# Optimization experiments

Measured on AMD Instinct MI355X. Metric: run time of the kernel, lower is better.

The kernel has to match this reference:

```python
import jax, jax.numpy as jnp
import numpy as np

N_G, E_G, E_H, E_I = 100000, 1000000, 1500000, 2000000
IN_FEATS = 64


def setup_inputs() -> dict:
    key = jax.random.key(0)
    ks = jax.random.split(key, 13)
    inp = {
        'z': jax.random.randint(ks[0], (N_G,), 0, 8),
        'src_g': jax.random.randint(ks[1], (E_G,), 0, N_G),
        'dst_g': jax.random.randint(ks[2], (E_G,), 0, N_G),
        'src_h': jax.random.randint(ks[3], (E_H,), 0, E_G),
        'dst_h': jax.random.randint(ks[4], (E_H,), 0, E_G),
        'src_i': jax.random.randint(ks[5], (E_I,), 0, E_H),
        'dst_i': jax.random.randint(ks[6], (E_I,), 0, E_H),
    }
    for n, k in zip(['e1', 'e2', 'e3', 'e4', 'e5', 'e6'], ks[7:13]):
        inp[n] = jax.random.normal(k, (2, IN_FEATS), dtype=jnp.float32)
    return inp


def reference(z, src_g, dst_g, src_h, dst_h, src_i, dst_i, e1, e2, e3, e4, e5, e6):
    # hop 1: g.apply_edges(send_z) -> per-edge endpoint labels, become h node data
    z_src = z[src_g]            # [E_G]
    z_dst = z[dst_g]            # [E_G]
    # hop 2: h.apply_edges(send_z2) -> become i node data
    z_src_src = z_src[src_h]    # [E_H]
    z_dst_dst = z_dst[dst_h]    # [E_H]
    # hop 3: i.apply_edges(comparison4) on edge endpoints of i
    za = z_src_src[src_i]       # [E_I]
    zb = z_src_src[dst_i]
    zc = z_dst_dst[src_i]
    zd = z_dst_dst[dst_i]
    zac = (za == zc).astype(jnp.int32)
    zab = (za == zb).astype(jnp.int32)
    zbc = (zc == zb).astype(jnp.int32)
    zad = (za == zd).astype(jnp.int32)
    zcd = (zc == zd).astype(jnp.int32)
    zbd = (zb == zd).astype(jnp.int32)
    # six 2-row embedding lookups summed -> [E_I, IN_FEATS]
    h = e1[zac] + e2[zab] + e3[zbc] + e4[zad] + e5[zcd] + e6[zbd]
    return h
```

## Files before the change

kernel.cpp:

```cpp
#include <hip/hip_runtime.h>


#define N_FEAT 64
#define WEPB   4096

typedef float f4 __attribute__((ext_vector_type(4)));

__global__ void hop1_table_kernel(const int* __restrict__ z,
                                  const int* __restrict__ src_g,
                                  const int* __restrict__ dst_g,
                                  unsigned short* __restrict__ zg,
                                  const float* __restrict__ e1,
                                  const float* __restrict__ e2,
                                  const float* __restrict__ e3,
                                  const float* __restrict__ e4,
                                  const float* __restrict__ e5,
                                  const float* __restrict__ e6,
                                  float* __restrict__ table,
                                  int n) {
    int i  = blockIdx.x * blockDim.x + threadIdx.x;
    int n4 = n >> 2;
    if (i < n4) {
        int4 s = ((const int4*)src_g)[i];
        int4 d = ((const int4*)dst_g)[i];
        unsigned zs0 = (unsigned)z[s.x], zd0 = (unsigned)z[d.x];
        unsigned zs1 = (unsigned)z[s.y], zd1 = (unsigned)z[d.y];
        unsigned zs2 = (unsigned)z[s.z], zd2 = (unsigned)z[d.z];
        unsigned zs3 = (unsigned)z[s.w], zd3 = (unsigned)z[d.w];
        unsigned r0 = (zs0 & 0xffu) | ((zd0 & 0xffu) << 8)
                    | ((zs1 & 0xffu) << 16) | ((zd1 & 0xffu) << 24);
        unsigned r1 = (zs2 & 0xffu) | ((zd2 & 0xffu) << 8)
                    | ((zs3 & 0xffu) << 16) | ((zd3 & 0xffu) << 24);
        ((uint2*)zg)[i] = make_uint2(r0, r1);
    } else {
        int e = (n4 << 2) + (i - n4);
        if (e < n) {
            zg[e] = (unsigned short)(((unsigned)z[src_g[e]] & 0xffu)
                                   | (((unsigned)z[dst_g[e]] & 0xffu) << 8));
        }
    }
    if (blockIdx.x < 16) {
        int idx = blockIdx.x * 256 + threadIdx.x;
        int cmb = idx >> 6;
        int f   = idx & (N_FEAT - 1);
        float v = e1[((cmb >> 0) & 1) * N_FEAT + f];
        v      += e2[((cmb >> 1) & 1) * N_FEAT + f];
        v      += e3[((cmb >> 2) & 1) * N_FEAT + f];
        v      += e4[((cmb >> 3) & 1) * N_FEAT + f];
        v      += e5[((cmb >> 4) & 1) * N_FEAT + f];
        v      += e6[((cmb >> 5) & 1) * N_FEAT + f];
        table[idx] = v;
    }
}

__global__ void hop2_kernel(const unsigned short* __restrict__ zg,
                            const int* __restrict__ src_h,
                            const int* __restrict__ dst_h,
                            unsigned short* __restrict__ zh,
                            int n) {
    int i  = blockIdx.x * blockDim.x + threadIdx.x;
    int n4 = n >> 2;
    if (i < n4) {
        int4 s = ((const int4*)src_h)[i];
        int4 d = ((const int4*)dst_h)[i];
        unsigned a0 = zg[s.x], b0 = zg[d.x];
        unsigned a1 = zg[s.y], b1 = zg[d.y];
        unsigned a2 = zg[s.z], b2 = zg[d.z];
        unsigned a3 = zg[s.w], b3 = zg[d.w];
        unsigned r0 = (a0 & 0xffu) | (b0 & 0xff00u)
                    | ((a1 & 0xffu) << 16) | ((b1 & 0xff00u) << 16);
        unsigned r1 = (a2 & 0xffu) | (b2 & 0xff00u)
                    | ((a3 & 0xffu) << 16) | ((b3 & 0xff00u) << 16);
        ((uint2*)zh)[i] = make_uint2(r0, r1);
    } else {
        int e = (n4 << 2) + (i - n4);
        if (e < n) {
            unsigned a = zg[src_h[e]], b = zg[dst_h[e]];
            zh[e] = (unsigned short)((a & 0xffu) | (b & 0xff00u));
        }
    }
}

__device__ __forceinline__ unsigned combo6(unsigned p, unsigned q) {
    unsigned za = p & 0xffu, zc = p >> 8;
    unsigned zb = q & 0xffu, zd = q >> 8;
    return (unsigned)(za == zc)
         | ((unsigned)(za == zb) << 1)
         | ((unsigned)(zc == zb) << 2)
         | ((unsigned)(za == zd) << 3)
         | ((unsigned)(zc == zd) << 4)
         | ((unsigned)(zb == zd) << 5);
}

__global__ void combo_kernel(const unsigned short* __restrict__ zh,
                             const int* __restrict__ src_i,
                             const int* __restrict__ dst_i,
                             unsigned char* __restrict__ combo,
                             int n) {
    int i  = blockIdx.x * blockDim.x + threadIdx.x;
    int n4 = n >> 2;
    if (i < n4) {
        int4 s = ((const int4*)src_i)[i];
        int4 d = ((const int4*)dst_i)[i];
        unsigned p0 = zh[s.x], q0 = zh[d.x];
        unsigned p1 = zh[s.y], q1 = zh[d.y];
        unsigned p2 = zh[s.z], q2 = zh[d.z];
        unsigned p3 = zh[s.w], q3 = zh[d.w];
        unsigned c0 = combo6(p0, q0);
        unsigned c1 = combo6(p1, q1);
        unsigned c2 = combo6(p2, q2);
        unsigned c3 = combo6(p3, q3);
        ((unsigned*)combo)[i] = c0 | (c1 << 8) | (c2 << 16) | (c3 << 24);
    } else {
        int e = (n4 << 2) + (i - n4);
        if (e < n) combo[e] = (unsigned char)combo6(zh[src_i[e]], zh[dst_i[e]]);
    }
}

__global__ __launch_bounds__(256)
void write_kernel(const unsigned char* __restrict__ combo,
                  const float* __restrict__ table,
                  float* __restrict__ out,
                  int nEdges) {
    __shared__ f4 tbl[64 * 16];
    __shared__ unsigned char cmb[WEPB];
    const int tid = threadIdx.x;
    const long long e0 = (long long)blockIdx.x * WEPB;
    int nb = nEdges - (int)e0; if (nb > WEPB) nb = WEPB;

    {
        const unsigned* src = (const unsigned*)(combo + e0);
        unsigned*       dst = (unsigned*)cmb;
        int nw = (nb + 3) >> 2;
#pragma unroll
        for (int k = 0; k < WEPB / 4 / 256; ++k) {
            int idx = k * 256 + tid;
            if (idx < nw) dst[idx] = src[idx];
        }
    }
    const f4* t4 = (const f4*)table;
#pragma unroll
    for (int k = 0; k < 4; ++k)
        tbl[k * 256 + tid] = t4[k * 256 + tid];
    __syncthreads();

    const int  w      = tid >> 6;
    const int  lane   = tid & 63;
    const int  c      = lane & 15;
    const int  leBase = w * (WEPB / 4) + (lane >> 4);
    const long long fBase = e0 * 16 + (long long)w * (WEPB * 16 / 4) + lane;
    constexpr int ITER = WEPB * 16 / 4 / 64;

    if (nb == WEPB) {
#pragma unroll 4
        for (int i = 0; i < ITER; ++i) {
            int le = leBase + i * 4;
            ((f4*)out)[fBase + (long long)i * 64] = tbl[(int)cmb[le] * 16 + c];
        }
    } else {
        const long long total = (long long)nEdges * 16;
#pragma unroll 4
        for (int i = 0; i < ITER; ++i) {
            long long f = fBase + (long long)i * 64;
            if (f < total) {
                int le = leBase + i * 4;
                ((f4*)out)[f] = tbl[(int)cmb[le] * 16 + c];
            }
        }
    }
}

extern "C" void kernel_launch(void* const* d_in, const int* in_sizes, int n_in,
                              void* d_out, int out_size, void* d_ws, size_t ws_size,
                              hipStream_t stream) {
    const int* z     = (const int*)d_in[0];
    const int* src_g = (const int*)d_in[1];
    const int* dst_g = (const int*)d_in[2];
    const int* src_h = (const int*)d_in[3];
    const int* dst_h = (const int*)d_in[4];
    const int* src_i = (const int*)d_in[5];
    const int* dst_i = (const int*)d_in[6];
    const float* e1  = (const float*)d_in[7];
    const float* e2  = (const float*)d_in[8];
    const float* e3  = (const float*)d_in[9];
    const float* e4  = (const float*)d_in[10];
    const float* e5  = (const float*)d_in[11];
    const float* e6  = (const float*)d_in[12];

    int E_G = in_sizes[1];
    int E_H = in_sizes[3];
    int E_I = in_sizes[5];

    char* ws = (char*)d_ws;
    float* table = (float*)ws;
    size_t off   = 64 * N_FEAT * sizeof(float);
    unsigned short* zg = (unsigned short*)(ws + off);
    off += (size_t)E_G * sizeof(unsigned short);
    off  = (off + 255) & ~(size_t)255;
    unsigned short* zh = (unsigned short*)(ws + off);
    off += (size_t)E_H * sizeof(unsigned short);
    off  = (off + 255) & ~(size_t)255;
    unsigned char* combo = (unsigned char*)(ws + off);

    float* out = (float*)d_out;

    {
        int n4 = E_G >> 2, nth = n4 + (E_G - (n4 << 2));
        int blocks = (nth + 255) / 256;
        if (blocks < 16) blocks = 16;
        hop1_table_kernel<<<blocks, 256, 0, stream>>>(z, src_g, dst_g, zg,
                                                      e1, e2, e3, e4, e5, e6,
                                                      table, E_G);
    }
    {
        int n4 = E_H >> 2, nth = n4 + (E_H - (n4 << 2));
        hop2_kernel<<<(nth + 255) / 256, 256, 0, stream>>>(zg, src_h, dst_h, zh, E_H);
    }
    {
        int n4 = E_I >> 2, nth = n4 + (E_I - (n4 << 2));
        combo_kernel<<<(nth + 255) / 256, 256, 0, stream>>>(zh, src_i, dst_i, combo, E_I);
    }
    {
        int blocks = (E_I + WEPB - 1) / WEPB;
        write_kernel<<<blocks, 256, 0, stream>>>(combo, table, out, E_I);
    }
}
```

Measured before the change: 148.6 us.

## Fuse combo computation into output write kernel and widen hop kernels to 8 edges

```diff
diff --git a/kernel.cpp b/kernel.cpp
--- a/kernel.cpp
+++ b/kernel.cpp
@@ -19,21 +19,23 @@
                                   float* __restrict__ table,
                                   int n) {
     int i  = blockIdx.x * blockDim.x + threadIdx.x;
-    int n4 = n >> 2;
-    if (i < n4) {
-        int4 s = ((const int4*)src_g)[i];
-        int4 d = ((const int4*)dst_g)[i];
-        unsigned zs0 = (unsigned)z[s.x], zd0 = (unsigned)z[d.x];
-        unsigned zs1 = (unsigned)z[s.y], zd1 = (unsigned)z[d.y];
-        unsigned zs2 = (unsigned)z[s.z], zd2 = (unsigned)z[d.z];
-        unsigned zs3 = (unsigned)z[s.w], zd3 = (unsigned)z[d.w];
-        unsigned r0 = (zs0 & 0xffu) | ((zd0 & 0xffu) << 8)
-                    | ((zs1 & 0xffu) << 16) | ((zd1 & 0xffu) << 24);
-        unsigned r1 = (zs2 & 0xffu) | ((zd2 & 0xffu) << 8)
-                    | ((zs3 & 0xffu) << 16) | ((zd3 & 0xffu) << 24);
-        ((uint2*)zg)[i] = make_uint2(r0, r1);
-    } else {
-        int e = (n4 << 2) + (i - n4);
+    int n8 = n >> 3;
+    if (i < n8) {
+        const int4* s4 = (const int4*)src_g;
+        const int4* d4 = (const int4*)dst_g;
+        int4 sa = s4[2 * i], sb = s4[2 * i + 1];
+        int4 da = d4[2 * i], db = d4[2 * i + 1];
+        unsigned r0 = ((unsigned)z[sa.x] & 0xffu) | (((unsigned)z[da.x] & 0xffu) << 8)
+                    | (((unsigned)z[sa.y] & 0xffu) << 16) | (((unsigned)z[da.y] & 0xffu) << 24);
+        unsigned r1 = ((unsigned)z[sa.z] & 0xffu) | (((unsigned)z[da.z] & 0xffu) << 8)
+                    | (((unsigned)z[sa.w] & 0xffu) << 16) | (((unsigned)z[da.w] & 0xffu) << 24);
+        unsigned r2 = ((unsigned)z[sb.x] & 0xffu) | (((unsigned)z[db.x] & 0xffu) << 8)
+                    | (((unsigned)z[sb.y] & 0xffu) << 16) | (((unsigned)z[db.y] & 0xffu) << 24);
+        unsigned r3 = ((unsigned)z[sb.z] & 0xffu) | (((unsigned)z[db.z] & 0xffu) << 8)
+                    | (((unsigned)z[sb.w] & 0xffu) << 16) | (((unsigned)z[db.w] & 0xffu) << 24);
+        ((uint4*)zg)[i] = make_uint4(r0, r1, r2, r3);
+    } else {
+        int e = (n8 << 3) + (i - n8);
         if (e < n) {
             zg[e] = (unsigned short)(((unsigned)z[src_g[e]] & 0xffu)
                                    | (((unsigned)z[dst_g[e]] & 0xffu) << 8));
@@ -59,21 +61,27 @@
                             unsigned short* __restrict__ zh,
                             int n) {
     int i  = blockIdx.x * blockDim.x + threadIdx.x;
-    int n4 = n >> 2;
-    if (i < n4) {
-        int4 s = ((const int4*)src_h)[i];
-        int4 d = ((const int4*)dst_h)[i];
-        unsigned a0 = zg[s.x], b0 = zg[d.x];
-        unsigned a1 = zg[s.y], b1 = zg[d.y];
-        unsigned a2 = zg[s.z], b2 = zg[d.z];
-        unsigned a3 = zg[s.w], b3 = zg[d.w];
-        unsigned r0 = (a0 & 0xffu) | (b0 & 0xff00u)
-                    | ((a1 & 0xffu) << 16) | ((b1 & 0xff00u) << 16);
-        unsigned r1 = (a2 & 0xffu) | (b2 & 0xff00u)
-                    | ((a3 & 0xffu) << 16) | ((b3 & 0xff00u) << 16);
-        ((uint2*)zh)[i] = make_uint2(r0, r1);
-    } else {
-        int e = (n4 << 2) + (i - n4);
+    int n8 = n >> 3;
+    if (i < n8) {
+        const int4* s4 = (const int4*)src_h;
+        const int4* d4 = (const int4*)dst_h;
+        int4 sa = s4[2 * i], sb = s4[2 * i + 1];
+        int4 da = d4[2 * i], db = d4[2 * i + 1];
+        unsigned a0 = zg[sa.x], b0 = zg[da.x];
+        unsigned a1 = zg[sa.y], b1 = zg[da.y];
+        unsigned a2 = zg[sa.z], b2 = zg[da.z];
+        unsigned a3 = zg[sa.w], b3 = zg[da.w];
+        unsigned a4 = zg[sb.x], b4 = zg[db.x];
+        unsigned a5 = zg[sb.y], b5 = zg[db.y];
+        unsigned a6 = zg[sb.z], b6 = zg[db.z];
+        unsigned a7 = zg[sb.w], b7 = zg[db.w];
+        unsigned r0 = (a0 & 0xffu) | (b0 & 0xff00u) | ((a1 & 0xffu) << 16) | ((b1 & 0xff00u) << 16);
+        unsigned r1 = (a2 & 0xffu) | (b2 & 0xff00u) | ((a3 & 0xffu) << 16) | ((b3 & 0xff00u) << 16);
+        unsigned r2 = (a4 & 0xffu) | (b4 & 0xff00u) | ((a5 & 0xffu) << 16) | ((b5 & 0xff00u) << 16);
+        unsigned r3 = (a6 & 0xffu) | (b6 & 0xff00u) | ((a7 & 0xffu) << 16) | ((b7 & 0xff00u) << 16);
+        ((uint4*)zh)[i] = make_uint4(r0, r1, r2, r3);
+    } else {
+        int e = (n8 << 3) + (i - n8);
         if (e < n) {
             unsigned a = zg[src_h[e]], b = zg[dst_h[e]];
             zh[e] = (unsigned short)((a & 0xffu) | (b & 0xff00u));
@@ -92,58 +100,63 @@
          | ((unsigned)(zb == zd) << 5);
 }
 
-__global__ void combo_kernel(const unsigned short* __restrict__ zh,
-                             const int* __restrict__ src_i,
-                             const int* __restrict__ dst_i,
-                             unsigned char* __restrict__ combo,
-                             int n) {
-    int i  = blockIdx.x * blockDim.x + threadIdx.x;
-    int n4 = n >> 2;
-    if (i < n4) {
-        int4 s = ((const int4*)src_i)[i];
-        int4 d = ((const int4*)dst_i)[i];
-        unsigned p0 = zh[s.x], q0 = zh[d.x];
-        unsigned p1 = zh[s.y], q1 = zh[d.y];
-        unsigned p2 = zh[s.z], q2 = zh[d.z];
-        unsigned p3 = zh[s.w], q3 = zh[d.w];
-        unsigned c0 = combo6(p0, q0);
-        unsigned c1 = combo6(p1, q1);
-        unsigned c2 = combo6(p2, q2);
-        unsigned c3 = combo6(p3, q3);
-        ((unsigned*)combo)[i] = c0 | (c1 << 8) | (c2 << 16) | (c3 << 24);
-    } else {
-        int e = (n4 << 2) + (i - n4);
-        if (e < n) combo[e] = (unsigned char)combo6(zh[src_i[e]], zh[dst_i[e]]);
-    }
-}
-
 __global__ __launch_bounds__(256)
-void write_kernel(const unsigned char* __restrict__ combo,
-                  const float* __restrict__ table,
-                  float* __restrict__ out,
-                  int nEdges) {
-    __shared__ f4 tbl[64 * 16];
-    __shared__ unsigned char cmb[WEPB];
+void fused_k3_kernel(const unsigned short* __restrict__ zh,
+                     const int* __restrict__ src_i,
+                     const int* __restrict__ dst_i,
+                     const float* __restrict__ table,
+                     float* __restrict__ out,
+                     int nEdges) {
+    __shared__ f4   tbl[64 * 16];
+    __shared__ uint4 cmbv[WEPB / 16];
     const int tid = threadIdx.x;
     const long long e0 = (long long)blockIdx.x * WEPB;
     int nb = nEdges - (int)e0; if (nb > WEPB) nb = WEPB;
 
-    {
-        const unsigned* src = (const unsigned*)(combo + e0);
-        unsigned*       dst = (unsigned*)cmb;
-        int nw = (nb + 3) >> 2;
-#pragma unroll
-        for (int k = 0; k < WEPB / 4 / 256; ++k) {
-            int idx = k * 256 + tid;
-            if (idx < nw) dst[idx] = src[idx];
-        }
-    }
     const f4* t4 = (const f4*)table;
 #pragma unroll
     for (int k = 0; k < 4; ++k)
         tbl[k * 256 + tid] = t4[k * 256 + tid];
+
+    if (nb == WEPB) {
+        const int4* si = (const int4*)(src_i + e0);
+        const int4* di = (const int4*)(dst_i + e0);
+        int4 s0 = si[tid * 4 + 0], s1 = si[tid * 4 + 1],
+             s2 = si[tid * 4 + 2], s3 = si[tid * 4 + 3];
+        int4 d0 = di[tid * 4 + 0], d1 = di[tid * 4 + 1],
+             d2 = di[tid * 4 + 2], d3 = di[tid * 4 + 3];
+        unsigned r0 =  combo6(zh[s0.x], zh[d0.x])
+                    | (combo6(zh[s0.y], zh[d0.y]) << 8)
+                    | (combo6(zh[s0.z], zh[d0.z]) << 16)
+                    | (combo6(zh[s0.w], zh[d0.w]) << 24);
+        unsigned r1 =  combo6(zh[s1.x], zh[d1.x])
+                    | (combo6(zh[s1.y], zh[d1.y]) << 8)
+                    | (combo6(zh[s1.z], zh[d1.z]) << 16)
+                    | (combo6(zh[s1.w], zh[d1.w]) << 24);
+        unsigned r2 =  combo6(zh[s2.x], zh[d2.x])
+                    | (combo6(zh[s2.y], zh[d2.y]) << 8)
+                    | (combo6(zh[s2.z], zh[d2.z]) << 16)
+                    | (combo6(zh[s2.w], zh[d2.w]) << 24);
+        unsigned r3 =  combo6(zh[s3.x], zh[d3.x])
+                    | (combo6(zh[s3.y], zh[d3.y]) << 8)
+                    | (combo6(zh[s3.z], zh[d3.z]) << 16)
+                    | (combo6(zh[s3.w], zh[d3.w]) << 24);
+        cmbv[tid] = make_uint4(r0, r1, r2, r3);
+    } else {
+        unsigned r[4] = {0u, 0u, 0u, 0u};
+        for (int j = 0; j < 16; ++j) {
+            int le = tid * 16 + j;
+            if (le < nb) {
+                long long e = e0 + le;
+                unsigned c = combo6(zh[src_i[e]], zh[dst_i[e]]);
+                r[j >> 2] |= c << ((j & 3) * 8);
+            }
+        }
+        cmbv[tid] = make_uint4(r[0], r[1], r[2], r[3]);
+    }
     __syncthreads();
 
+    const unsigned char* cmb = (const unsigned char*)cmbv;
     const int  w      = tid >> 6;
     const int  lane   = tid & 63;
     const int  c      = lane & 15;
@@ -198,14 +211,11 @@
     off += (size_t)E_G * sizeof(unsigned short);
     off  = (off + 255) & ~(size_t)255;
     unsigned short* zh = (unsigned short*)(ws + off);
-    off += (size_t)E_H * sizeof(unsigned short);
-    off  = (off + 255) & ~(size_t)255;
-    unsigned char* combo = (unsigned char*)(ws + off);
 
     float* out = (float*)d_out;
 
     {
-        int n4 = E_G >> 2, nth = n4 + (E_G - (n4 << 2));
+        int n8 = E_G >> 3, nth = n8 + (E_G - (n8 << 3));
         int blocks = (nth + 255) / 256;
         if (blocks < 16) blocks = 16;
         hop1_table_kernel<<<blocks, 256, 0, stream>>>(z, src_g, dst_g, zg,
@@ -213,15 +223,11 @@
                                                       table, E_G);
     }
     {
-        int n4 = E_H >> 2, nth = n4 + (E_H - (n4 << 2));
+        int n8 = E_H >> 3, nth = n8 + (E_H - (n8 << 3));
         hop2_kernel<<<(nth + 255) / 256, 256, 0, stream>>>(zg, src_h, dst_h, zh, E_H);
-    }
-    {
-        int n4 = E_I >> 2, nth = n4 + (E_I - (n4 << 2));
-        combo_kernel<<<(nth + 255) / 256, 256, 0, stream>>>(zh, src_i, dst_i, combo, E_I);
     }
     {
         int blocks = (E_I + WEPB - 1) / WEPB;
-        write_kernel<<<blocks, 256, 0, stream>>>(combo, table, out, E_I);
-    }
-}
+        fused_k3_kernel<<<blocks, 256, 0, stream>>>(zh, src_i, dst_i, table, out, E_I);
+    }
+}
```

New measurement: 141.7 us, median of 2. 4.7% less time.
